# Kernel tuning notes

Measured on AMD Instinct MI355X. Metric: run time of the kernel, lower is better.

## Reference

```python
import jax, jax.numpy as jnp
import numpy as np

NUM_NODES = 50000
NUM_HYPEREDGES = 50000
NNZ = 800000
IN_CH, HID_CH, OUT_CH = 512, 256, 64


def setup_inputs() -> dict:
    key = jax.random.key(0)
    k = jax.random.split(key, 6)
    x = jax.random.normal(k[0], (NUM_NODES, IN_CH), dtype=jnp.float32)
    node_idx = jax.random.randint(k[1], (NNZ,), 0, NUM_NODES)
    hedge_idx = jax.random.randint(k[2], (NNZ,), 0, NUM_HYPEREDGES)
    edge_index = jnp.stack([node_idx, hedge_idx]).astype(jnp.int64)
    W1 = jax.random.normal(k[3], (IN_CH, HID_CH), dtype=jnp.float32) * (1.0 / np.sqrt(IN_CH))
    b1 = jnp.zeros((HID_CH,), dtype=jnp.float32)
    W2 = jax.random.normal(k[4], (HID_CH, OUT_CH), dtype=jnp.float32) * (1.0 / np.sqrt(HID_CH))
    b2 = jnp.zeros((OUT_CH,), dtype=jnp.float32)
    return {"x": x, "edge_index": edge_index, "W1": W1, "b1": b1, "W2": W2, "b2": b2}


def hypergraph_conv(x, node_idx, hedge_idx, W, b):
    # x' = D^{-1} H B^{-1} H^T (x Theta) + b   (PyG HypergraphConv, unit edge weights)
    h = x @ W                                   # [N, F_out]
    ones = jnp.ones(node_idx.shape[0], dtype=x.dtype)
    D = jax.ops.segment_sum(ones, node_idx, num_segments=NUM_NODES)        # node degree
    B = jax.ops.segment_sum(ones, hedge_idx, num_segments=NUM_HYPEREDGES)  # hyperedge degree
    D_inv = jnp.where(D > 0, 1.0 / D, 0.0)
    B_inv = jnp.where(B > 0, 1.0 / B, 0.0)
    # node -> hyperedge aggregation
    m = jax.ops.segment_sum(h[node_idx], hedge_idx, num_segments=NUM_HYPEREDGES)
    m = m * B_inv[:, None]                      # [E, F_out]
    # hyperedge -> node aggregation
    out = jax.ops.segment_sum(m[hedge_idx], node_idx, num_segments=NUM_NODES)
    out = out * D_inv[:, None]                  # [N, F_out]
    return out + b


def reference(x, edge_index, W1, b1, W2, b2):
    node_idx = edge_index[0]
    hedge_idx = edge_index[1]
    h = hypergraph_conv(x, node_idx, hedge_idx, W1, b1)
    h = jax.nn.relu(h)
    h = hypergraph_conv(h, node_idx, hedge_idx, W2, b2)
    return jax.nn.log_softmax(h, axis=1)
```

## Files before the change

### kernel.cpp

```cpp
#include <hip/hip_runtime.h>
#include <math.h>

#define N_NODES  50000
#define N_HEDGES 50000
#define NNZ_     800000
#define IN_CH    512
#define HID_CH   256
#define OUT_CH   64
#define M_PAD    50048
#define NBK      391

#define BH_BLK   98
#define PKW1_BLK 16
#define PK2_BLK  64

typedef __attribute__((ext_vector_type(8))) short bf16x8;
typedef __attribute__((ext_vector_type(4))) float f32x4;

__device__ __forceinline__ unsigned short f2bf(float f) {
    union { float f; unsigned u; } v; v.f = f;
    unsigned r = v.u + 0x7FFFu + ((v.u >> 16) & 1u);
    return (unsigned short)(r >> 16);
}
__device__ __forceinline__ float bf2f(unsigned short u) {
    union { unsigned u; float f; } v; v.u = (unsigned)u << 16; return v.f;
}

#define GLL16(g, l)                                                            \
    __builtin_amdgcn_global_load_lds(                                          \
        (const __attribute__((address_space(1))) void*)(g),                    \
        (__attribute__((address_space(3))) void*)(l), 16, 0, 0)

__global__ void prep_kernel(const float* __restrict__ W1, unsigned short* __restrict__ Wp1,
                            const float* __restrict__ W2, unsigned short* __restrict__ Wp2,
                            const int* __restrict__ ni, const int* __restrict__ hi,
                            int* __restrict__ cnts) {
    const int blk = blockIdx.x;
    const int t = threadIdx.x;
    __shared__ float smf[256 * 33];
    if (blk < BH_BLK) {
        int* lh = (int*)smf;
        int* ln = lh + NBK;
        for (int k = t; k < NBK; k += 256) { lh[k] = 0; ln[k] = 0; }
        __syncthreads();
        for (int i4 = blk * 256 + t; i4 < NNZ_ / 4; i4 += BH_BLK * 256) {
            const int4 nv = *(const int4*)(ni + i4 * 4);
            const int4 hv = *(const int4*)(hi + i4 * 4);
            atomicAdd(&ln[nv.x >> 7], 1); atomicAdd(&ln[nv.y >> 7], 1);
            atomicAdd(&ln[nv.z >> 7], 1); atomicAdd(&ln[nv.w >> 7], 1);
            atomicAdd(&lh[hv.x >> 7], 1); atomicAdd(&lh[hv.y >> 7], 1);
            atomicAdd(&lh[hv.z >> 7], 1); atomicAdd(&lh[hv.w >> 7], 1);
        }
        __syncthreads();
        for (int k = t; k < NBK; k += 256) {
            if (lh[k]) atomicAdd(&cnts[k], lh[k]);
            if (ln[k]) atomicAdd(&cnts[400 + k], ln[k]);
        }
    } else if (blk < BH_BLK + PKW1_BLK) {
        const int kt = blk - BH_BLK;
        #pragma unroll 4
        for (int r = 0; r < 32; ++r)
            smf[t * 33 + r] = W1[(size_t)(kt * 32 + r) * HID_CH + t];
        __syncthreads();
        unsigned short* dst = Wp1 + kt * 8192;
        #pragma unroll
        for (int rep = 0; rep < 4; ++rep) {
            const int it = rep * 256 + t;
            const int n = it >> 2, o = it & 3;
            const float* src = &smf[n * 33 + o * 8];
            ushort4 w0, w1;
            w0.x = f2bf(src[0]); w0.y = f2bf(src[1]);
            w0.z = f2bf(src[2]); w0.w = f2bf(src[3]);
            w1.x = f2bf(src[4]); w1.y = f2bf(src[5]);
            w1.z = f2bf(src[6]); w1.w = f2bf(src[7]);
            *(ushort4*)(dst + n * 32 + o * 8) = w0;
            *(ushort4*)(dst + n * 32 + o * 8 + 4) = w1;
        }
    } else {
        const int i = (blk - (BH_BLK + PKW1_BLK)) * 256 + t;
        const int kt = i / (OUT_CH * 32);
        const int r  = i % (OUT_CH * 32);
        const int n  = r >> 5, kk = r & 31;
        Wp2[i] = f2bf(W2[(size_t)(kt * 32 + kk) * OUT_CH + n]);
    }
}

__global__ void bin_kernel(const int* __restrict__ ni, const int* __restrict__ hi,
                           int* __restrict__ cnts,
                           int* __restrict__ bstartH, int* __restrict__ bstartN,
                           unsigned* __restrict__ recN, unsigned* __restrict__ recH) {
    __shared__ int sA[512], sB[512];
    __shared__ int offH[NBK + 1], offN[NBK + 1];
    __shared__ int cH[NBK], cN[NBK], bH[NBK], bN[NBK];
    const int t = threadIdx.x;
    int* relH = cnts + 800;
    int* relN = cnts + 1200;

    int vH = 0, vN = 0;
    if (t < 512) { vH = (t < NBK) ? cnts[t] : 0; sA[t] = vH; }
    else { const int tt = t - 512; vN = (tt < NBK) ? cnts[400 + tt] : 0; sB[tt] = vN; }
    __syncthreads();
    #pragma unroll
    for (int d = 1; d < 512; d <<= 1) {
        int u = 0;
        if (t < 512) { if (t >= d) u = sA[t - d]; }
        else { const int tt = t - 512; if (tt >= d) u = sB[tt - d]; }
        __syncthreads();
        if (t < 512) sA[t] += u; else sB[t - 512] += u;
        __syncthreads();
    }
    if (t < NBK) offH[t] = sA[t] - vH;
    if (t >= 512 && t - 512 < NBK) offN[t - 512] = sB[t - 512] - vN;
    if (t == NBK - 1) offH[NBK] = sA[t];
    if (t - 512 == NBK - 1) offN[NBK] = sB[t - 512];
    __syncthreads();
    if (blockIdx.x == 0) {
        for (int i = t; i <= NBK; i += 1024) {
            bstartH[i] = offH[i];
            bstartN[i] = offN[i];
        }
    }

    for (int k = t; k < NBK; k += 1024) { cH[k] = 0; cN[k] = 0; }
    __syncthreads();
    const int gid = blockIdx.x * 1024 + t;
    const int i0 = gid * 4;
    int4 nv, hv;
    const bool act = (i0 < NNZ_);
    if (act) {
        nv = *(const int4*)(ni + i0);
        hv = *(const int4*)(hi + i0);
        atomicAdd(&cN[nv.x >> 7], 1); atomicAdd(&cN[nv.y >> 7], 1);
        atomicAdd(&cN[nv.z >> 7], 1); atomicAdd(&cN[nv.w >> 7], 1);
        atomicAdd(&cH[hv.x >> 7], 1); atomicAdd(&cH[hv.y >> 7], 1);
        atomicAdd(&cH[hv.z >> 7], 1); atomicAdd(&cH[hv.w >> 7], 1);
    }
    __syncthreads();
    for (int k = t; k < NBK; k += 1024) {
        bH[k] = cH[k] ? offH[k] + atomicAdd(&relH[k], cH[k]) : 0;
        bN[k] = cN[k] ? offN[k] + atomicAdd(&relN[k], cN[k]) : 0;
    }
    __syncthreads();
    for (int k = t; k < NBK; k += 1024) { cH[k] = bH[k]; cN[k] = bN[k]; }
    __syncthreads();
    if (act) {
        int nn[4] = {nv.x, nv.y, nv.z, nv.w};
        int hh[4] = {hv.x, hv.y, hv.z, hv.w};
        #pragma unroll
        for (int k = 0; k < 4; ++k) {
            int p = atomicAdd(&cH[hh[k] >> 7], 1);
            recH[p] = ((unsigned)(hh[k] & 127) << 16) | (unsigned)nn[k];
            p = atomicAdd(&cN[nn[k] >> 7], 1);
            recN[p] = ((unsigned)(nn[k] & 127) << 16) | (unsigned)hh[k];
        }
    }
}

__global__ void buildcsr_kernel(const int* __restrict__ bstartH, const unsigned* __restrict__ recH,
                                int* __restrict__ offH, int* __restrict__ colH,
                                float* __restrict__ Binv,
                                const int* __restrict__ bstartN, const unsigned* __restrict__ recN,
                                int* __restrict__ offN, int* __restrict__ colN,
                                float* __restrict__ Dinv) {
    int b = blockIdx.x;
    const int* bstart; const unsigned* rec; int* off; int* col; float* inv;
    if (b < NBK) { bstart = bstartH; rec = recH; off = offH; col = colH; inv = Binv; }
    else { b -= NBK; bstart = bstartN; rec = recN; off = offN; col = colN; inv = Dinv; }
    const int s = bstart[b], e = bstart[b + 1];
    const int t = threadIdx.x;
    __shared__ int lc[128], ps[128], cur[128];
    if (t < 128) lc[t] = 0;
    __syncthreads();
    for (int i = s + t; i < e; i += 256) atomicAdd(&lc[rec[i] >> 16], 1);
    __syncthreads();
    if (t < 128) ps[t] = lc[t];
    __syncthreads();
    #pragma unroll
    for (int d = 1; d < 128; d <<= 1) {
        int v = (t >= d && t < 128) ? ps[t - d] : 0;
        __syncthreads();
        if (t < 128) ps[t] += v;
        __syncthreads();
    }
    if (t < 128) {
        const int excl = s + ps[t] - lc[t];
        cur[t] = excl;
        const int id = b * 128 + t;
        if (id < N_NODES) {
            off[id] = excl;
            inv[id] = lc[t] > 0 ? 1.f / (float)lc[t] : 0.f;
        }
    }
    if (b == NBK - 1 && t == 255) off[N_NODES] = bstart[NBK];
    __syncthreads();
    for (int i = s + t; i < e; i += 256) {
        const unsigned r = rec[i];
        const int p = atomicAdd(&cur[r >> 16], 1);
        col[p] = (int)(r & 0xFFFFu);
    }
}

__global__ void gemm1_fused_kernel(const float* __restrict__ X,
                                   const unsigned short* __restrict__ Wp,
                                   unsigned short* __restrict__ C, int M) {
    constexpr int BM = 64, BN = 256, K = IN_CH, KT = K / 32;
    __shared__ unsigned short As[BM * 32];
    __shared__ unsigned short Bs[BN * 32];
    const int tid  = threadIdx.x;
    const int wave = tid >> 6;
    const int lane = tid & 63;
    const int wr = wave >> 1;
    const int wc = wave & 1;
    const int quad = lane >> 4;
    const int l15  = lane & 15;
    const int row0 = blockIdx.x * BM;

    float4 va[2];
    auto loadA = [&](int kt) {
        #pragma unroll
        for (int r = 0; r < 2; ++r) {
            const int idx = r * 256 + tid;
            const int row = idx >> 3;
            const int kc  = (idx & 7) * 4;
            const int gr  = row0 + row;
            float4 v = make_float4(0.f, 0.f, 0.f, 0.f);
            if (gr < M) v = *(const float4*)(X + (size_t)gr * K + kt * 32 + kc);
            va[r] = v;
        }
    };

    f32x4 acc[2][8];
    #pragma unroll
    for (int mt = 0; mt < 2; ++mt)
        #pragma unroll
        for (int nt = 0; nt < 8; ++nt)
            acc[mt][nt] = (f32x4)0.f;

    loadA(0);
    for (int kt = 0; kt < KT; ++kt) {
        __syncthreads();
        #pragma unroll
        for (int r = 0; r < 2; ++r) {
            const int idx = r * 256 + tid;
            const int row = idx >> 3;
            const int kc  = (idx & 7) * 4;
            ushort4 o;
            o.x = f2bf(va[r].x); o.y = f2bf(va[r].y);
            o.z = f2bf(va[r].z); o.w = f2bf(va[r].w);
            *(ushort4*)(As + row * 32 + kc) = o;
        }
        const size_t bk = (size_t)kt * BN * 32;
        #pragma unroll
        for (int r = 0; r < 4; ++r)
            GLL16(Wp + bk + r * 2048 + (size_t)tid * 8, Bs + r * 2048 + tid * 8);
        __syncthreads();
        if (kt + 1 < KT) loadA(kt + 1);

        bf16x8 af[2], bfr[8];
        #pragma unroll
        for (int mt = 0; mt < 2; ++mt)
            af[mt] = *(const bf16x8*)(As + (wr * 32 + mt * 16 + l15) * 32 + quad * 8);
        #pragma unroll
        for (int nt = 0; nt < 8; ++nt)
            bfr[nt] = *(const bf16x8*)(Bs + (wc * 128 + nt * 16 + l15) * 32 + quad * 8);
        #pragma unroll
        for (int mt = 0; mt < 2; ++mt)
            #pragma unroll
            for (int nt = 0; nt < 8; ++nt)
                acc[mt][nt] = __builtin_amdgcn_mfma_f32_16x16x32_bf16(
                    af[mt], bfr[nt], acc[mt][nt], 0, 0, 0);
    }

    #pragma unroll
    for (int mt = 0; mt < 2; ++mt) {
        const int gr0 = row0 + wr * 32 + mt * 16 + quad * 4;
        #pragma unroll
        for (int nt = 0; nt < 8; ++nt) {
            const int gc = wc * 128 + nt * 16 + l15;
            #pragma unroll
            for (int r = 0; r < 4; ++r) {
                const int gr = gr0 + r;
                if (gr < M) C[(size_t)gr * HID_CH + gc] = f2bf(acc[mt][nt][r]);
            }
        }
    }
}

template <int BN>
__global__ void mfma_gemm_kernel(const unsigned short* __restrict__ A,
                                 const unsigned short* __restrict__ Wp,
                                 unsigned short* __restrict__ C, int M, int N, int K) {
    constexpr int NT = BN / 32;
    __shared__ unsigned short As[128 * 32];
    __shared__ unsigned short Bs[BN * 32];

    const int tid  = threadIdx.x;
    const int wave = tid >> 6;
    const int lane = tid & 63;
    const int wr = wave >> 1;
    const int wc = wave & 1;
    const int quad = lane >> 4;
    const int l15  = lane & 15;
    const int row0 = blockIdx.y * 128;
    const int col0 = blockIdx.x * BN;

    const size_t a_g0   = (size_t)(row0 + wave * 16 + (lane >> 2)) * K + (lane & 3) * 8;
    const int    a_l0   = (wave * 16 + (lane >> 2)) * 32 + (lane & 3) * 8;
    const size_t b_gbase = ((size_t)col0 + wave * 16 + (lane >> 2)) * 32 + (lane & 3) * 8;
    const int    b_l0   = (wave * 16 + (lane >> 2)) * 32 + (lane & 3) * 8;

    f32x4 acc[4][NT];
    #pragma unroll
    for (int mt = 0; mt < 4; ++mt)
        #pragma unroll
        for (int nt = 0; nt < NT; ++nt)
            acc[mt][nt] = (f32x4)0.f;

    const int KT = K / 32;
    for (int kt = 0; kt < KT; ++kt) {
        __syncthreads();
        GLL16(A + a_g0 + (size_t)kt * 32, As + a_l0);
        GLL16(A + a_g0 + (size_t)(kt * 32) + (size_t)64 * K, As + a_l0 + 64 * 32);
        const size_t bk = (size_t)kt * N * 32;
        GLL16(Wp + bk + b_gbase, Bs + b_l0);
        if (BN == 128)
            GLL16(Wp + bk + b_gbase + 64 * 32, Bs + b_l0 + 64 * 32);
        __syncthreads();

        bf16x8 af[4], bf[NT];
        #pragma unroll
        for (int mt = 0; mt < 4; ++mt)
            af[mt] = *(const bf16x8*)(As + (wr * 64 + mt * 16 + l15) * 32 + quad * 8);
        #pragma unroll
        for (int nt = 0; nt < NT; ++nt)
            bf[nt] = *(const bf16x8*)(Bs + (wc * (BN / 2) + nt * 16 + l15) * 32 + quad * 8);
        #pragma unroll
        for (int mt = 0; mt < 4; ++mt)
            #pragma unroll
            for (int nt = 0; nt < NT; ++nt)
                acc[mt][nt] = __builtin_amdgcn_mfma_f32_16x16x32_bf16(
                    af[mt], bf[nt], acc[mt][nt], 0, 0, 0);
    }

    #pragma unroll
    for (int mt = 0; mt < 4; ++mt) {
        const int gr0 = row0 + wr * 64 + mt * 16 + quad * 4;
        #pragma unroll
        for (int nt = 0; nt < NT; ++nt) {
            const int gc = col0 + wc * (BN / 2) + nt * 16 + l15;
            #pragma unroll
            for (int r = 0; r < 4; ++r) {
                int gr = gr0 + r;
                if (gr < M) C[(size_t)gr * N + gc] = f2bf(acc[mt][nt][r]);
            }
        }
    }
}

template <bool EPI>
__global__ void gather256_kernel(const unsigned short* __restrict__ src,
                                 unsigned short* __restrict__ dst,
                                 const int* __restrict__ off, const int* __restrict__ col,
                                 const float* __restrict__ scale,
                                 const float* __restrict__ bias, int nrows) {
    int row = blockIdx.x * (blockDim.x >> 6) + (threadIdx.x >> 6);
    if (row >= nrows) return;
    const int lane = threadIdx.x & 63;
    const int g = lane >> 5;
    const int l = lane & 31;
    const int s = off[row], e = off[row + 1];
    float a[8];
    #pragma unroll
    for (int k = 0; k < 8; ++k) a[k] = 0.f;
    int j = s + g;
    for (; j + 6 < e; j += 8) {
        const bf16x8 u0 = *(const bf16x8*)(src + ((size_t)col[j]     << 8) + (l << 3));
        const bf16x8 u1 = *(const bf16x8*)(src + ((size_t)col[j + 2] << 8) + (l << 3));
        const bf16x8 u2 = *(const bf16x8*)(src + ((size_t)col[j + 4] << 8) + (l << 3));
        const bf16x8 u3 = *(const bf16x8*)(src + ((size_t)col[j + 6] << 8) + (l << 3));
        #pragma unroll
        for (int k = 0; k < 8; ++k)
            a[k] += (bf2f((unsigned short)u0[k]) + bf2f((unsigned short)u1[k])) +
                    (bf2f((unsigned short)u2[k]) + bf2f((unsigned short)u3[k]));
    }
    for (; j < e; j += 2) {
        const bf16x8 u = *(const bf16x8*)(src + ((size_t)col[j] << 8) + (l << 3));
        #pragma unroll
        for (int k = 0; k < 8; ++k) a[k] += bf2f((unsigned short)u[k]);
    }
    #pragma unroll
    for (int k = 0; k < 8; ++k) a[k] += __shfl_xor(a[k], 32);
    if (g != 0) return;
    const float sc = scale[row];
    float v[8];
    #pragma unroll
    for (int k = 0; k < 8; ++k) v[k] = a[k] * sc;
    if (EPI) {
        const float4 b0 = *(const float4*)(bias + (l << 3));
        const float4 b1 = *(const float4*)(bias + (l << 3) + 4);
        v[0] = fmaxf(v[0] + b0.x, 0.f); v[1] = fmaxf(v[1] + b0.y, 0.f);
        v[2] = fmaxf(v[2] + b0.z, 0.f); v[3] = fmaxf(v[3] + b0.w, 0.f);
        v[4] = fmaxf(v[4] + b1.x, 0.f); v[5] = fmaxf(v[5] + b1.y, 0.f);
        v[6] = fmaxf(v[6] + b1.z, 0.f); v[7] = fmaxf(v[7] + b1.w, 0.f);
    }
    bf16x8 o;
    #pragma unroll
    for (int k = 0; k < 8; ++k) o[k] = (short)f2bf(v[k]);
    *(bf16x8*)(dst + ((size_t)row << 8) + (l << 3)) = o;
}

template <bool LSM>
__global__ void gather64_kernel(const unsigned short* __restrict__ src, void* __restrict__ dstv,
                                const int* __restrict__ off, const int* __restrict__ col,
                                const float* __restrict__ scale,
                                const float* __restrict__ bias, int nrows) {
    int row = blockIdx.x * (blockDim.x >> 6) + (threadIdx.x >> 6);
    if (row >= nrows) return;
    const int lane = threadIdx.x & 63;
    const int g = lane >> 3;
    const int l = lane & 7;
    const int s = off[row], e = off[row + 1];
    float a[8];
    #pragma unroll
    for (int k = 0; k < 8; ++k) a[k] = 0.f;
    int j = s + g;
    for (; j + 8 < e; j += 16) {
        const bf16x8 u0 = *(const bf16x8*)(src + ((size_t)col[j]     << 6) + (l << 3));
        const bf16x8 u1 = *(const bf16x8*)(src + ((size_t)col[j + 8] << 6) + (l << 3));
        #pragma unroll
        for (int k = 0; k < 8; ++k)
            a[k] += bf2f((unsigned short)u0[k]) + bf2f((unsigned short)u1[k]);
    }
    if (j < e) {
        const bf16x8 u = *(const bf16x8*)(src + ((size_t)col[j] << 6) + (l << 3));
        #pragma unroll
        for (int k = 0; k < 8; ++k) a[k] += bf2f((unsigned short)u[k]);
    }
    #pragma unroll
    for (int k = 0; k < 8; ++k) {
        a[k] += __shfl_xor(a[k], 8);
        a[k] += __shfl_xor(a[k], 16);
        a[k] += __shfl_xor(a[k], 32);
    }
    const float sc = scale[row];
    float v[8];
    #pragma unroll
    for (int k = 0; k < 8; ++k) v[k] = a[k] * sc;
    if (LSM) {
        const float4 b0 = *(const float4*)(bias + (l << 3));
        const float4 b1 = *(const float4*)(bias + (l << 3) + 4);
        v[0] += b0.x; v[1] += b0.y; v[2] += b0.z; v[3] += b0.w;
        v[4] += b1.x; v[5] += b1.y; v[6] += b1.z; v[7] += b1.w;
        float m = v[0];
        #pragma unroll
        for (int k = 1; k < 8; ++k) m = fmaxf(m, v[k]);
        m = fmaxf(m, __shfl_xor(m, 1));
        m = fmaxf(m, __shfl_xor(m, 2));
        m = fmaxf(m, __shfl_xor(m, 4));
        float su = 0.f;
        #pragma unroll
        for (int k = 0; k < 8; ++k) su += expf(v[k] - m);
        su += __shfl_xor(su, 1);
        su += __shfl_xor(su, 2);
        su += __shfl_xor(su, 4);
        const float lg = m + logf(su);
        if (g == 0) {
            float* dp = (float*)dstv + (size_t)row * OUT_CH + (l << 3);
            float4 o0, o1;
            o0.x = v[0] - lg; o0.y = v[1] - lg; o0.z = v[2] - lg; o0.w = v[3] - lg;
            o1.x = v[4] - lg; o1.y = v[5] - lg; o1.z = v[6] - lg; o1.w = v[7] - lg;
            *(float4*)dp = o0;
            *(float4*)(dp + 4) = o1;
        }
    } else if (g == 0) {
        bf16x8 o;
        #pragma unroll
        for (int k = 0; k < 8; ++k) o[k] = (short)f2bf(v[k]);
        *(bf16x8*)((unsigned short*)dstv + (size_t)row * OUT_CH + (l << 3)) = o;
    }
}

extern "C" void kernel_launch(void* const* d_in, const int* in_sizes, int n_in,
                              void* d_out, int out_size, void* d_ws, size_t ws_size,
                              hipStream_t stream) {
    const float* x  = (const float*)d_in[0];
    const int*   ei = (const int*)d_in[1];
    const float* W1 = (const float*)d_in[2];
    const float* b1 = (const float*)d_in[3];
    const float* W2 = (const float*)d_in[4];
    const float* b2 = (const float*)d_in[5];
    float* out = (float*)d_out;

    const int* node_idx  = ei;
    const int* hedge_idx = ei + NNZ_;

    const size_t RCAP = (size_t)M_PAD * IN_CH / 2;
    float* regionA = (float*)d_ws;
    float* regionB = regionA + RCAP;
    float* Dinv = regionB + RCAP;
    float* Binv = Dinv + N_NODES;
    int* offN = (int*)(Binv + N_HEDGES);
    int* offH = offN + N_NODES + 1;
    int* colN = offH + N_HEDGES + 1;
    int* colH = colN + NNZ_;
    unsigned short* Wp1 = (unsigned short*)(colH + NNZ_);
    unsigned short* Wp2 = Wp1 + IN_CH * HID_CH;
    int* cnts    = (int*)(Wp2 + HID_CH * OUT_CH);
    int* bstartH = cnts + 1600;
    int* bstartN = bstartH + 400;

    unsigned* recH = (unsigned*)regionA;
    unsigned* recN = recH + NNZ_;

    unsigned short* h1_bf = (unsigned short*)regionA;
    unsigned short* m1_bf = (unsigned short*)regionB;
    unsigned short* h2_bf = (unsigned short*)regionA;
    unsigned short* g_bf  = (unsigned short*)regionB;
    unsigned short* m2_bf = (unsigned short*)regionB + (size_t)M_PAD * OUT_CH;

    hipMemsetAsync(cnts, 0, 1600 * sizeof(int), stream);
    prep_kernel<<<BH_BLK + PKW1_BLK + PK2_BLK, 256, 0, stream>>>(
        W1, Wp1, W2, Wp2, node_idx, hedge_idx, cnts);
    bin_kernel<<<200, 1024, 0, stream>>>(node_idx, hedge_idx, cnts,
                                         bstartH, bstartN, recN, recH);
    buildcsr_kernel<<<2 * NBK, 256, 0, stream>>>(bstartH, recH, offH, colH, Binv,
                                                 bstartN, recN, offN, colN, Dinv);

    gemm1_fused_kernel<<<(N_NODES + 63) / 64, 256, 0, stream>>>(x, Wp1, h1_bf, N_NODES);
    gather256_kernel<false><<<(N_HEDGES + 3) / 4, 256, 0, stream>>>(
        h1_bf, m1_bf, offH, colH, Binv, nullptr, N_HEDGES);
    gather256_kernel<true><<<(N_NODES + 3) / 4, 256, 0, stream>>>(
        m1_bf, h2_bf, offN, colN, Dinv, b1, N_NODES);

    mfma_gemm_kernel<64><<<dim3(OUT_CH / 64, (N_NODES + 127) / 128), 256, 0, stream>>>(
        h2_bf, Wp2, g_bf, N_NODES, OUT_CH, HID_CH);
    gather64_kernel<false><<<(N_HEDGES + 3) / 4, 256, 0, stream>>>(
        g_bf, m2_bf, offH, colH, Binv, nullptr, N_HEDGES);
    gather64_kernel<true><<<(N_NODES + 3) / 4, 256, 0, stream>>>(
        m2_bf, out, offN, colN, Dinv, b2, N_NODES);
}
```

Baseline: 387.2 us.

## Merge CSR build into first GEMM launch as extra blocks

Folds the CSR construction work into the first GEMM launch by appending 2*NBK extra blocks that take a separate branch, so the dense GEMM and the bucket-local CSR build run concurrently instead of as two serial launches. The bin records move out of regionA into their own workspace slot, because the GEMM now writes h1 into regionA while those records are still being read. This removes one kernel launch and the idle tail between launches. In exchange the CSR branch reuses the GEMM's shared buffers, the combined kernel may carry higher register pressure, and the workspace needs more room.

```diff
diff --git a/kernel.cpp b/kernel.cpp
--- a/kernel.cpp
+++ b/kernel.cpp
@@ -9,6 +9,7 @@
 #define OUT_CH   64
 #define M_PAD    50048
 #define NBK      391
+#define G1_BLKS  ((N_NODES + 63) / 64)
 
 #define BH_BLK   98
 #define PKW1_BLK 16
@@ -156,59 +157,63 @@
     }
 }
 
-__global__ void buildcsr_kernel(const int* __restrict__ bstartH, const unsigned* __restrict__ recH,
-                                int* __restrict__ offH, int* __restrict__ colH,
-                                float* __restrict__ Binv,
-                                const int* __restrict__ bstartN, const unsigned* __restrict__ recN,
-                                int* __restrict__ offN, int* __restrict__ colN,
-                                float* __restrict__ Dinv) {
-    int b = blockIdx.x;
-    const int* bstart; const unsigned* rec; int* off; int* col; float* inv;
-    if (b < NBK) { bstart = bstartH; rec = recH; off = offH; col = colH; inv = Binv; }
-    else { b -= NBK; bstart = bstartN; rec = recN; off = offN; col = colN; inv = Dinv; }
-    const int s = bstart[b], e = bstart[b + 1];
-    const int t = threadIdx.x;
-    __shared__ int lc[128], ps[128], cur[128];
-    if (t < 128) lc[t] = 0;
-    __syncthreads();
-    for (int i = s + t; i < e; i += 256) atomicAdd(&lc[rec[i] >> 16], 1);
-    __syncthreads();
-    if (t < 128) ps[t] = lc[t];
-    __syncthreads();
-    #pragma unroll
-    for (int d = 1; d < 128; d <<= 1) {
-        int v = (t >= d && t < 128) ? ps[t - d] : 0;
-        __syncthreads();
-        if (t < 128) ps[t] += v;
-        __syncthreads();
-    }
-    if (t < 128) {
-        const int excl = s + ps[t] - lc[t];
-        cur[t] = excl;
-        const int id = b * 128 + t;
-        if (id < N_NODES) {
-            off[id] = excl;
-            inv[id] = lc[t] > 0 ? 1.f / (float)lc[t] : 0.f;
-        }
-    }
-    if (b == NBK - 1 && t == 255) off[N_NODES] = bstart[NBK];
-    __syncthreads();
-    for (int i = s + t; i < e; i += 256) {
-        const unsigned r = rec[i];
-        const int p = atomicAdd(&cur[r >> 16], 1);
-        col[p] = (int)(r & 0xFFFFu);
-    }
-}
-
-__global__ void gemm1_fused_kernel(const float* __restrict__ X,
-                                   const unsigned short* __restrict__ Wp,
-                                   unsigned short* __restrict__ C, int M) {
+__global__ void gemm1_csr_kernel(const float* __restrict__ X,
+                                 const unsigned short* __restrict__ Wp,
+                                 unsigned short* __restrict__ C, int M,
+                                 const int* __restrict__ bstartH, const unsigned* __restrict__ recH,
+                                 int* __restrict__ offH, int* __restrict__ colH,
+                                 float* __restrict__ Binv,
+                                 const int* __restrict__ bstartN, const unsigned* __restrict__ recN,
+                                 int* __restrict__ offN, int* __restrict__ colN,
+                                 float* __restrict__ Dinv) {
     constexpr int BM = 64, BN = 256, K = IN_CH, KT = K / 32;
     __shared__ unsigned short As[BM * 32];
     __shared__ unsigned short Bs[BN * 32];
-    const int tid  = threadIdx.x;
-    const int wave = tid >> 6;
-    const int lane = tid & 63;
+    const int t = threadIdx.x;
+
+    if (blockIdx.x >= G1_BLKS) {
+        int b = blockIdx.x - G1_BLKS;
+        const int* bstart; const unsigned* rec; int* off; int* col; float* inv;
+        if (b < NBK) { bstart = bstartH; rec = recH; off = offH; col = colH; inv = Binv; }
+        else { b -= NBK; bstart = bstartN; rec = recN; off = offN; col = colN; inv = Dinv; }
+        const int s = bstart[b], e = bstart[b + 1];
+        int* lc  = (int*)As;
+        int* ps  = lc + 128;
+        int* cur = ps + 128;
+        if (t < 128) lc[t] = 0;
+        __syncthreads();
+        for (int i = s + t; i < e; i += 256) atomicAdd(&lc[rec[i] >> 16], 1);
+        __syncthreads();
+        if (t < 128) ps[t] = lc[t];
+        __syncthreads();
+        #pragma unroll
+        for (int d = 1; d < 128; d <<= 1) {
+            int v = (t >= d && t < 128) ? ps[t - d] : 0;
+            __syncthreads();
+            if (t < 128) ps[t] += v;
+            __syncthreads();
+        }
+        if (t < 128) {
+            const int excl = s + ps[t] - lc[t];
+            cur[t] = excl;
+            const int id = b * 128 + t;
+            if (id < N_NODES) {
+                off[id] = excl;
+                inv[id] = lc[t] > 0 ? 1.f / (float)lc[t] : 0.f;
+            }
+        }
+        if (b == NBK - 1 && t == 255) off[N_NODES] = bstart[NBK];
+        __syncthreads();
+        for (int i = s + t; i < e; i += 256) {
+            const unsigned r = rec[i];
+            const int p = atomicAdd(&cur[r >> 16], 1);
+            col[p] = (int)(r & 0xFFFFu);
+        }
+        return;
+    }
+
+    const int wave = t >> 6;
+    const int lane = t & 63;
     const int wr = wave >> 1;
     const int wc = wave & 1;
     const int quad = lane >> 4;
@@ -219,7 +224,7 @@
     auto loadA = [&](int kt) {
         #pragma unroll
         for (int r = 0; r < 2; ++r) {
-            const int idx = r * 256 + tid;
+            const int idx = r * 256 + t;
             const int row = idx >> 3;
             const int kc  = (idx & 7) * 4;
             const int gr  = row0 + row;
@@ -241,7 +246,7 @@
         __syncthreads();
         #pragma unroll
         for (int r = 0; r < 2; ++r) {
-            const int idx = r * 256 + tid;
+            const int idx = r * 256 + t;
             const int row = idx >> 3;
             const int kc  = (idx & 7) * 4;
             ushort4 o;
@@ -252,7 +257,7 @@
         const size_t bk = (size_t)kt * BN * 32;
         #pragma unroll
         for (int r = 0; r < 4; ++r)
-            GLL16(Wp + bk + r * 2048 + (size_t)tid * 8, Bs + r * 2048 + tid * 8);
+            GLL16(Wp + bk + r * 2048 + (size_t)t * 8, Bs + r * 2048 + t * 8);
         __syncthreads();
         if (kt + 1 < KT) loadA(kt + 1);
 
@@ -508,8 +513,7 @@
     int* cnts    = (int*)(Wp2 + HID_CH * OUT_CH);
     int* bstartH = cnts + 1600;
     int* bstartN = bstartH + 400;
-
-    unsigned* recH = (unsigned*)regionA;
+    unsigned* recH = (unsigned*)(bstartN + 400);
     unsigned* recN = recH + NNZ_;
 
     unsigned short* h1_bf = (unsigned short*)regionA;
@@ -523,10 +527,12 @@
         W1, Wp1, W2, Wp2, node_idx, hedge_idx, cnts);
     bin_kernel<<<200, 1024, 0, stream>>>(node_idx, hedge_idx, cnts,
                                          bstartH, bstartN, recN, recH);
-    buildcsr_kernel<<<2 * NBK, 256, 0, stream>>>(bstartH, recH, offH, colH, Binv,
-                                                 bstartN, recN, offN, colN, Dinv);
-
-    gemm1_fused_kernel<<<(N_NODES + 63) / 64, 256, 0, stream>>>(x, Wp1, h1_bf, N_NODES);
+
+    gemm1_csr_kernel<<<G1_BLKS + 2 * NBK, 256, 0, stream>>>(
+        x, Wp1, h1_bf, N_NODES,
+        bstartH, recH, offH, colH, Binv,
+        bstartN, recN, offN, colN, Dinv);
+
     gather256_kernel<false><<<(N_HEDGES + 3) / 4, 256, 0, stream>>>(
         h1_bf, m1_bf, offH, colH, Binv, nullptr, N_HEDGES);
     gather256_kernel<true><<<(N_NODES + 3) / 4, 256, 0, stream>>>(
```

Result: no change. 390.8 us (+0.9%).

## Fuse second-layer W2 projection into node gather epilogue, drop separate GEMM

Applied to the files above, without the earlier changes.

The node-side gather of layer 1 now applies bias and ReLU, then multiplies the 256-wide row by W2 inside the same wavefront using shuffles and scalar FMAs, writing the 64-wide g directly. This removes the h2 write and read round trip and a separate MFMA GEMM launch. The CSR record scratch is moved out of regionA so it no longer aliases buffers. The cost is per-row scalar dot products (256x64 FMAs per node with shuffles), replacing tensor-core MFMA work with ALU work and repeated W2 loads from cache.

```diff
diff --git a/kernel.cpp b/kernel.cpp
--- a/kernel.cpp
+++ b/kernel.cpp
@@ -7,7 +7,6 @@
 #define IN_CH    512
 #define HID_CH   256
 #define OUT_CH   64
-#define M_PAD    50048
 #define NBK      391
 
 #define BH_BLK   98
@@ -286,83 +285,10 @@
     }
 }
 
-template <int BN>
-__global__ void mfma_gemm_kernel(const unsigned short* __restrict__ A,
-                                 const unsigned short* __restrict__ Wp,
-                                 unsigned short* __restrict__ C, int M, int N, int K) {
-    constexpr int NT = BN / 32;
-    __shared__ unsigned short As[128 * 32];
-    __shared__ unsigned short Bs[BN * 32];
-
-    const int tid  = threadIdx.x;
-    const int wave = tid >> 6;
-    const int lane = tid & 63;
-    const int wr = wave >> 1;
-    const int wc = wave & 1;
-    const int quad = lane >> 4;
-    const int l15  = lane & 15;
-    const int row0 = blockIdx.y * 128;
-    const int col0 = blockIdx.x * BN;
-
-    const size_t a_g0   = (size_t)(row0 + wave * 16 + (lane >> 2)) * K + (lane & 3) * 8;
-    const int    a_l0   = (wave * 16 + (lane >> 2)) * 32 + (lane & 3) * 8;
-    const size_t b_gbase = ((size_t)col0 + wave * 16 + (lane >> 2)) * 32 + (lane & 3) * 8;
-    const int    b_l0   = (wave * 16 + (lane >> 2)) * 32 + (lane & 3) * 8;
-
-    f32x4 acc[4][NT];
-    #pragma unroll
-    for (int mt = 0; mt < 4; ++mt)
-        #pragma unroll
-        for (int nt = 0; nt < NT; ++nt)
-            acc[mt][nt] = (f32x4)0.f;
-
-    const int KT = K / 32;
-    for (int kt = 0; kt < KT; ++kt) {
-        __syncthreads();
-        GLL16(A + a_g0 + (size_t)kt * 32, As + a_l0);
-        GLL16(A + a_g0 + (size_t)(kt * 32) + (size_t)64 * K, As + a_l0 + 64 * 32);
-        const size_t bk = (size_t)kt * N * 32;
-        GLL16(Wp + bk + b_gbase, Bs + b_l0);
-        if (BN == 128)
-            GLL16(Wp + bk + b_gbase + 64 * 32, Bs + b_l0 + 64 * 32);
-        __syncthreads();
-
-        bf16x8 af[4], bf[NT];
-        #pragma unroll
-        for (int mt = 0; mt < 4; ++mt)
-            af[mt] = *(const bf16x8*)(As + (wr * 64 + mt * 16 + l15) * 32 + quad * 8);
-        #pragma unroll
-        for (int nt = 0; nt < NT; ++nt)
-            bf[nt] = *(const bf16x8*)(Bs + (wc * (BN / 2) + nt * 16 + l15) * 32 + quad * 8);
-        #pragma unroll
-        for (int mt = 0; mt < 4; ++mt)
-            #pragma unroll
-            for (int nt = 0; nt < NT; ++nt)
-                acc[mt][nt] = __builtin_amdgcn_mfma_f32_16x16x32_bf16(
-                    af[mt], bf[nt], acc[mt][nt], 0, 0, 0);
-    }
-
-    #pragma unroll
-    for (int mt = 0; mt < 4; ++mt) {
-        const int gr0 = row0 + wr * 64 + mt * 16 + quad * 4;
-        #pragma unroll
-        for (int nt = 0; nt < NT; ++nt) {
-            const int gc = col0 + wc * (BN / 2) + nt * 16 + l15;
-            #pragma unroll
-            for (int r = 0; r < 4; ++r) {
-                int gr = gr0 + r;
-                if (gr < M) C[(size_t)gr * N + gc] = f2bf(acc[mt][nt][r]);
-            }
-        }
-    }
-}
-
-template <bool EPI>
 __global__ void gather256_kernel(const unsigned short* __restrict__ src,
                                  unsigned short* __restrict__ dst,
                                  const int* __restrict__ off, const int* __restrict__ col,
-                                 const float* __restrict__ scale,
-                                 const float* __restrict__ bias, int nrows) {
+                                 const float* __restrict__ scale, int nrows) {
     int row = blockIdx.x * (blockDim.x >> 6) + (threadIdx.x >> 6);
     if (row >= nrows) return;
     const int lane = threadIdx.x & 63;
@@ -392,21 +318,62 @@
     for (int k = 0; k < 8; ++k) a[k] += __shfl_xor(a[k], 32);
     if (g != 0) return;
     const float sc = scale[row];
+    bf16x8 o;
+    #pragma unroll
+    for (int k = 0; k < 8; ++k) o[k] = (short)f2bf(a[k] * sc);
+    *(bf16x8*)(dst + ((size_t)row << 8) + (l << 3)) = o;
+}
+
+__global__ void gather256_w2_kernel(const unsigned short* __restrict__ src,
+                                    unsigned short* __restrict__ g,
+                                    const int* __restrict__ off, const int* __restrict__ col,
+                                    const float* __restrict__ scale,
+                                    const float* __restrict__ bias,
+                                    const unsigned short* __restrict__ Wp2, int nrows) {
+    int row = blockIdx.x * (blockDim.x >> 6) + (threadIdx.x >> 6);
+    if (row >= nrows) return;
+    const int lane = threadIdx.x & 63;
+    const int gq = lane >> 5;
+    const int l = lane & 31;
+    const int s = off[row], e = off[row + 1];
+    float a[8];
+    #pragma unroll
+    for (int k = 0; k < 8; ++k) a[k] = 0.f;
+    int j = s + gq;
+    for (; j + 6 < e; j += 8) {
+        const bf16x8 u0 = *(const bf16x8*)(src + ((size_t)col[j]     << 8) + (l << 3));
+        const bf16x8 u1 = *(const bf16x8*)(src + ((size_t)col[j + 2] << 8) + (l << 3));
+        const bf16x8 u2 = *(const bf16x8*)(src + ((size_t)col[j + 4] << 8) + (l << 3));
+        const bf16x8 u3 = *(const bf16x8*)(src + ((size_t)col[j + 6] << 8) + (l << 3));
+        #pragma unroll
+        for (int k = 0; k < 8; ++k)
+            a[k] += (bf2f((unsigned short)u0[k]) + bf2f((unsigned short)u1[k])) +
+                    (bf2f((unsigned short)u2[k]) + bf2f((unsigned short)u3[k]));
+    }
+    for (; j < e; j += 2) {
+        const bf16x8 u = *(const bf16x8*)(src + ((size_t)col[j] << 8) + (l << 3));
+        #pragma unroll
+        for (int k = 0; k < 8; ++k) a[k] += bf2f((unsigned short)u[k]);
+    }
+    #pragma unroll
+    for (int k = 0; k < 8; ++k) a[k] += __shfl_xor(a[k], 32);
+    const float sc = scale[row];
+    const float4 b0 = *(const float4*)(bias + (l << 3));
+    const float4 b1v = *(const float4*)(bias + (l << 3) + 4);
     float v[8];
-    #pragma unroll
-    for (int k = 0; k < 8; ++k) v[k] = a[k] * sc;
-    if (EPI) {
-        const float4 b0 = *(const float4*)(bias + (l << 3));
-        const float4 b1 = *(const float4*)(bias + (l << 3) + 4);
-        v[0] = fmaxf(v[0] + b0.x, 0.f); v[1] = fmaxf(v[1] + b0.y, 0.f);
-        v[2] = fmaxf(v[2] + b0.z, 0.f); v[3] = fmaxf(v[3] + b0.w, 0.f);
-        v[4] = fmaxf(v[4] + b1.x, 0.f); v[5] = fmaxf(v[5] + b1.y, 0.f);
-        v[6] = fmaxf(v[6] + b1.z, 0.f); v[7] = fmaxf(v[7] + b1.w, 0.f);
-    }
-    bf16x8 o;
-    #pragma unroll
-    for (int k = 0; k < 8; ++k) o[k] = (short)f2bf(v[k]);
-    *(bf16x8*)(dst + ((size_t)row << 8) + (l << 3)) = o;
+    v[0] = fmaxf(a[0] * sc + b0.x, 0.f); v[1] = fmaxf(a[1] * sc + b0.y, 0.f);
+    v[2] = fmaxf(a[2] * sc + b0.z, 0.f); v[3] = fmaxf(a[3] * sc + b0.w, 0.f);
+    v[4] = fmaxf(a[4] * sc + b1v.x, 0.f); v[5] = fmaxf(a[5] * sc + b1v.y, 0.f);
+    v[6] = fmaxf(a[6] * sc + b1v.z, 0.f); v[7] = fmaxf(a[7] * sc + b1v.w, 0.f);
+    float acc = 0.f;
+    #pragma unroll 4
+    for (int sl = 0; sl < 32; ++sl) {
+        const bf16x8 w = *(const bf16x8*)(Wp2 + (sl >> 2) * 2048 + (lane << 5) + ((sl & 3) << 3));
+        #pragma unroll
+        for (int k = 0; k < 8; ++k)
+            acc += __shfl(v[k], sl) * bf2f((unsigned short)w[k]);
+    }
+    g[(size_t)row * OUT_CH + lane] = f2bf(acc);
 }
 
 template <bool LSM>
@@ -494,7 +461,7 @@
     const int* node_idx  = ei;
     const int* hedge_idx = ei + NNZ_;
 
-    const size_t RCAP = (size_t)M_PAD * IN_CH / 2;
+    const size_t RCAP = (size_t)50048 * IN_CH / 2;
     float* regionA = (float*)d_ws;
     float* regionB = regionA + RCAP;
     float* Dinv = regionB + RCAP;
@@ -508,15 +475,13 @@
     int* cnts    = (int*)(Wp2 + HID_CH * OUT_CH);
     int* bstartH = cnts + 1600;
     int* bstartN = bstartH + 400;
-
-    unsigned* recH = (unsigned*)regionA;
+    unsigned* recH = (unsigned*)(bstartN + 400);
     unsigned* recN = recH + NNZ_;
 
     unsigned short* h1_bf = (unsigned short*)regionA;
     unsigned short* m1_bf = (unsigned short*)regionB;
-    unsigned short* h2_bf = (unsigned short*)regionA;
-    unsigned short* g_bf  = (unsigned short*)regionB;
-    unsigned short* m2_bf = (unsigned short*)regionB + (size_t)M_PAD * OUT_CH;
+    unsigned short* g_bf  = (unsigned short*)regionA;
+    unsigned short* m2_bf = (unsigned short*)regionB + (size_t)50048 * OUT_CH;
 
     hipMemsetAsync(cnts, 0, 1600 * sizeof(int), stream);
     prep_kernel<<<BH_BLK + PKW1_BLK + PK2_BLK, 256, 0, stream>>>(
@@ -527,13 +492,11 @@
                                                  bstartN, recN, offN, colN, Dinv);
 
     gemm1_fused_kernel<<<(N_NODES + 63) / 64, 256, 0, stream>>>(x, Wp1, h1_bf, N_NODES);
-    gather256_kernel<false><<<(N_HEDGES + 3) / 4, 256, 0, stream>>>(
-        h1_bf, m1_bf, offH, colH, Binv, nullptr, N_HEDGES);
-    gather256_kernel<true><<<(N_NODES + 3) / 4, 256, 0, stream>>>(
-        m1_bf, h2_bf, offN, colN, Dinv, b1, N_NODES);
-
-    mfma_gemm_kernel<64><<<dim3(OUT_CH / 64, (N_NODES + 127) / 128), 256, 0, stream>>>(
-        h2_bf, Wp2, g_bf, N_NODES, OUT_CH, HID_CH);
+    gather256_kernel<<<(N_HEDGES + 3) / 4, 256, 0, stream>>>(
+        h1_bf, m1_bf, offH, colH, Binv, N_HEDGES);
+    gather256_w2_kernel<<<(N_NODES + 3) / 4, 256, 0, stream>>>(
+        m1_bf, g_bf, offN, colN, Dinv, b1, Wp2, N_NODES);
+
     gather64_kernel<false><<<(N_HEDGES + 3) / 4, 256, 0, stream>>>(
         g_bf, m2_bf, offH, colH, Binv, nullptr, N_HEDGES);
     gather64_kernel<true><<<(N_NODES + 3) / 4, 256, 0, stream>>>(
```

Result: slower. 470.7 us (+21.6%).
